# Optimization experiments

Measured on AMD Instinct MI355X. Metric: run time of the kernel, lower is better.

The kernel has to match this reference:

```python
import jax, jax.numpy as jnp
import numpy as np

N_HEADS = 16
ROPE_BASE = 10000.0


def _rope_tables(T, head_dim, dtype):
    inv_freq = 1.0 / (ROPE_BASE ** (jnp.arange(0, head_dim, 2, dtype=jnp.float32) / head_dim))
    t = jnp.arange(T, dtype=jnp.float32)
    freqs = jnp.outer(t, inv_freq)              # (T, head_dim/2)
    emb = jnp.concatenate([freqs, freqs], -1)   # (T, head_dim)
    return jnp.cos(emb).astype(dtype), jnp.sin(emb).astype(dtype)


def _rotate_half(x):
    x1, x2 = jnp.split(x, 2, axis=-1)
    return jnp.concatenate([-x2, x1], axis=-1)


def setup_inputs() -> dict:
    key = jax.random.key(0)
    k1, k2, k3 = jax.random.split(key, 3)
    B, T, C = 2, 2048, 2048
    x = jax.random.normal(k1, (B, T, C), dtype=jnp.float32)
    Wqkv = jax.random.normal(k2, (C, 3 * C), dtype=jnp.float32) * (1.0 / np.sqrt(C))
    Wproj = jax.random.normal(k3, (C, C), dtype=jnp.float32) * (1.0 / np.sqrt(C))
    return {"x": x, "Wqkv": Wqkv, "Wproj": Wproj}


def reference(x, Wqkv, Wproj):
    B, T, C = x.shape
    H = N_HEADS
    D = C // H
    qkv = jnp.einsum('btc,cd->btd', x, Wqkv)            # (B,T,3C)
    q, k, v = jnp.split(qkv, 3, axis=-1)
    # (B,T,C) -> (B,H,T,D)
    q = q.reshape(B, T, H, D).transpose(0, 2, 1, 3)
    k = k.reshape(B, T, H, D).transpose(0, 2, 1, 3)
    v = v.reshape(B, T, H, D).transpose(0, 2, 1, 3)
    cos, sin = _rope_tables(T, D, x.dtype)              # (T,D) each
    q = q * cos + _rotate_half(q) * sin
    k = k * cos + _rotate_half(k) * sin
    scale = 1.0 / jnp.sqrt(jnp.asarray(D, x.dtype))
    att = jnp.einsum('bhqd,bhkd->bhqk', q, k) * scale   # (B,H,T,T)
    causal = jnp.tril(jnp.ones((T, T), dtype=bool))
    att = jnp.where(causal, att, jnp.asarray(-jnp.inf, att.dtype))
    att = jax.nn.softmax(att, axis=-1)
    y = jnp.einsum('bhqk,bhkd->bhqd', att, v)           # (B,H,T,D)
    y = y.transpose(0, 2, 1, 3).reshape(B, T, C)
    return jnp.einsum('btc,cd->btd', y, Wproj)
```

## Files before the change

### kernel.cpp

```cpp
#include <hip/hip_runtime.h>
#include <stdint.h>

#define T_SEQ 2048
#define NH 16
#define HD 128
#define CC 2048
#define N3 6144
#define MM 4096

typedef short bf16x8 __attribute__((ext_vector_type(8)));
typedef float f32x4 __attribute__((ext_vector_type(4)));
typedef float f32x16 __attribute__((ext_vector_type(16)));
typedef unsigned int u32x4 __attribute__((ext_vector_type(4)));

__device__ __forceinline__ unsigned short f2bf(float f) {
  unsigned int u = __float_as_uint(f);
  u += 0x7FFF + ((u >> 16) & 1);
  return (unsigned short)(u >> 16);
}
__device__ __forceinline__ float bf2f(unsigned short h) {
  return __uint_as_float(((unsigned int)h) << 16);
}
__device__ __forceinline__ unsigned int cvt_pk_bf16(float lo, float hi) {
  unsigned int r;
  asm("v_cvt_pk_bf16_f32 %0, %1, %2" : "=v"(r) : "v"(lo), "v"(hi));
  return r;
}

__global__ __launch_bounds__(256) void k_transpose_cvt(const float* __restrict__ in,
                                                       unsigned short* __restrict__ out,
                                                       int K, int N) {
  __shared__ float tile[32][33];
  int k0 = blockIdx.x * 32;
  int n0 = blockIdx.y * 32;
  int tx = threadIdx.x & 31, ty = threadIdx.x >> 5;
  #pragma unroll
  for (int r = ty; r < 32; r += 8)
    tile[r][tx] = in[(size_t)(k0 + r) * N + n0 + tx];
  __syncthreads();
  #pragma unroll
  for (int r = ty; r < 32; r += 8)
    out[(size_t)(n0 + r) * K + k0 + tx] = f2bf(tile[tx][r]);
}

__global__ __launch_bounds__(256) void k_cvt(const float* __restrict__ in,
                                             unsigned short* __restrict__ out, int n4) {
  int i = blockIdx.x * 256 + threadIdx.x;
  if (i >= n4) return;
  float4 v = ((const float4*)in)[i];
  ushort4 o;
  o.x = f2bf(v.x); o.y = f2bf(v.y); o.z = f2bf(v.z); o.w = f2bf(v.w);
  ((ushort4*)out)[i] = o;
}

template<int NJ, int EPI, int MMAJ>
__global__ __launch_bounds__(512, 1) void k_gemm8(const unsigned short* __restrict__ A,
                                                  const unsigned short* __restrict__ Bt,
                                                  float* __restrict__ C,
                                                  unsigned short* __restrict__ qo,
                                                  unsigned short* __restrict__ ko,
                                                  unsigned short* __restrict__ vo,
                                                  int M, int N, int K) {
  constexpr int BU = NJ / 2;
  constexpr int DSTRIDE = (1 + BU) * 16384;
  extern __shared__ __align__(16) char lds[];
  const int tid = threadIdx.x;
  const int lane = tid & 63;
  const int lr = lane & 15, lg = lane >> 4;
  const int wave = tid >> 6;
  const int wm = wave >> 2, wn = wave & 3;
  const int nwg = gridDim.x;
  const int bid = blockIdx.x;
  const int wg = (bid & 7) * (nwg >> 3) + (bid >> 3);
  const int GX = M >> 7;
  const int GN = N / (NJ * 64);
  const int mt = MMAJ ? (wg % GX) : (wg / GN);
  const int nt = MMAJ ? (wg / GX) : (wg % GN);
  const int m0 = mt * 128, n0 = nt * NJ * 64;
  const int NT = K >> 6;

  auto STAGE = [&](int d, int op, int h, int t) {
    const unsigned short* src = op ? Bt : A;
    const int r0 = (op ? n0 + h * 128 : m0);
    const int kc = t * 64;
    char* base = lds + d * DSTRIDE + op * 16384 + h * 16384;
    #pragma unroll
    for (int l = 0; l < 2; ++l) {
      int p = (l * 512 + tid) * 16;
      int qq = p ^ (((p >> 7) & 7) << 4);
      const unsigned short* g = src + (size_t)(r0 + (qq >> 7)) * K + kc + ((qq & 127) >> 1);
      __builtin_amdgcn_global_load_lds(
          (const __attribute__((address_space(1))) void*)g,
          (__attribute__((address_space(3))) void*)(base + (l * 512 + (tid & 448)) * 16),
          16, 0, 0);
    }
  };
  auto RD = [&](int d, int op, int row, int kb) -> bf16x8 {
    const char* base = lds + d * DSTRIDE + op * 16384;
    int p = row * 128 + kb;
    p ^= ((p >> 7) & 7) << 4;
    return *(const bf16x8*)(base + p);
  };

  f32x4 acc[4][NJ];
  #pragma unroll
  for (int i = 0; i < 4; ++i)
    #pragma unroll
    for (int j = 0; j < NJ; ++j) acc[i][j] = (f32x4){0.f, 0.f, 0.f, 0.f};

  bf16x8 bfrg[NJ][2];

#define GPH(D, MI, READB, DOST, SD, SO, SH, ST, VM)                                      \
  {                                                                                      \
    if (READB) {                                                                         \
      _Pragma("unroll")                                                                  \
      for (int nj = 0; nj < NJ; ++nj)                                                    \
        _Pragma("unroll")                                                                \
        for (int ks = 0; ks < 2; ++ks)                                                   \
          bfrg[nj][ks] = RD(D, 1, wn * NJ * 16 + nj * 16 + lr, ks * 64 + lg * 16);       \
    }                                                                                    \
    bf16x8 af[2];                                                                        \
    _Pragma("unroll")                                                                    \
    for (int ks = 0; ks < 2; ++ks)                                                       \
      af[ks] = RD(D, 0, wm * 64 + (MI) * 16 + lr, ks * 64 + lg * 16);                    \
    if (DOST) STAGE(SD, SO, SH, ST);                                                     \
    __builtin_amdgcn_s_barrier();                                                        \
    asm volatile("s_waitcnt lgkmcnt(0)" ::: "memory");                                   \
    __builtin_amdgcn_s_setprio(1);                                                       \
    _Pragma("unroll")                                                                    \
    for (int nj = 0; nj < NJ; ++nj)                                                      \
      _Pragma("unroll")                                                                  \
      for (int ks = 0; ks < 2; ++ks)                                                     \
        acc[MI][nj] = __builtin_amdgcn_mfma_f32_16x16x32_bf16(af[ks], bfrg[nj][ks], acc[MI][nj], 0, 0, 0); \
    __builtin_amdgcn_s_setprio(0);                                                       \
    if ((VM) == 6) asm volatile("s_waitcnt vmcnt(6)" ::: "memory");                      \
    if ((VM) == 4) asm volatile("s_waitcnt vmcnt(4)" ::: "memory");                      \
    __builtin_amdgcn_s_barrier();                                                        \
  }

#define GPM(D, MIB, READB, VM, ...)                                                      \
  {                                                                                      \
    if (READB) {                                                                         \
      _Pragma("unroll")                                                                  \
      for (int nj = 0; nj < NJ; ++nj)                                                    \
        _Pragma("unroll")                                                                \
        for (int ks = 0; ks < 2; ++ks)                                                   \
          bfrg[nj][ks] = RD(D, 1, wn * NJ * 16 + nj * 16 + lr, ks * 64 + lg * 16);       \
    }                                                                                    \
    bf16x8 af2[2][2];                                                                    \
    _Pragma("unroll")                                                                    \
    for (int mm = 0; mm < 2; ++mm)                                                       \
      _Pragma("unroll")                                                                  \
      for (int ks = 0; ks < 2; ++ks)                                                     \
        af2[mm][ks] = RD(D, 0, wm * 64 + (MIB + mm) * 16 + lr, ks * 64 + lg * 16);       \
    __VA_ARGS__                                                                          \
    __builtin_amdgcn_s_barrier();                                                        \
    asm volatile("s_waitcnt lgkmcnt(0)" ::: "memory");                                   \
    __builtin_amdgcn_s_setprio(1);                                                       \
    _Pragma("unroll")                                                                    \
    for (int mm = 0; mm < 2; ++mm)                                                       \
      _Pragma("unroll")                                                                  \
      for (int nj = 0; nj < NJ; ++nj)                                                    \
        _Pragma("unroll")                                                                \
        for (int ks = 0; ks < 2; ++ks)                                                   \
          acc[MIB + mm][nj] = __builtin_amdgcn_mfma_f32_16x16x32_bf16(af2[mm][ks], bfrg[nj][ks], acc[MIB + mm][nj], 0, 0, 0); \
    __builtin_amdgcn_s_setprio(0);                                                       \
    if ((VM) == 4) asm volatile("s_waitcnt vmcnt(4)" ::: "memory");                      \
    if ((VM) == 2) asm volatile("s_waitcnt vmcnt(2)" ::: "memory");                      \
    __builtin_amdgcn_s_barrier();                                                        \
  }

  const int t1 = NT > 1 ? 1 : 0;
  #pragma unroll
  for (int h = 0; h < BU; ++h) STAGE(0, 1, h, 0);
  STAGE(0, 0, 0, 0);
  #pragma unroll
  for (int h = 0; h < BU; ++h) STAGE(1, 1, h, t1);
  if (NJ == 6) asm volatile("s_waitcnt vmcnt(6)" ::: "memory");
  else         asm volatile("s_waitcnt vmcnt(4)" ::: "memory");
  __builtin_amdgcn_s_barrier();

  for (int it = 0; it < (NT >> 1); ++it) {
    const int tb  = 2 * it + 1;
    const int ta1 = min(2 * it + 2, NT - 1);
    const int tb1 = min(2 * it + 3, NT - 1);
    if constexpr (NJ == 6) {
      GPH(0, 0, true,  true, 1, 0, 0, tb,  -1)
      GPH(0, 1, false, true, 0, 1, 0, ta1, -1)
      GPH(0, 2, false, true, 0, 1, 1, ta1, -1)
      GPH(0, 3, false, true, 0, 1, 2, ta1,  6)
      GPH(1, 0, true,  true, 0, 0, 0, ta1, -1)
      GPH(1, 1, false, true, 1, 1, 0, tb1, -1)
      GPH(1, 2, false, true, 1, 1, 1, tb1, -1)
      GPH(1, 3, false, true, 1, 1, 2, tb1,  6)
    } else {
      GPM(0, 0, true,  -1, STAGE(1, 0, 0, tb);)
      GPM(0, 2, false,  2, STAGE(0, 1, 0, ta1);)
      GPM(1, 0, true,  -1, STAGE(0, 1, 1, ta1); STAGE(0, 0, 0, ta1);)
      GPM(1, 2, false,  4, STAGE(1, 1, 0, tb1); STAGE(1, 1, 1, tb1);)
    }
  }
#undef GPH
#undef GPM

  #pragma unroll
  for (int mi = 0; mi < 4; ++mi) {
    #pragma unroll
    for (int nj = 0; nj < NJ; ++nj) {
      #pragma unroll
      for (int j = 0; j < 4; ++j) {
        int m = m0 + wm * 64 + mi * 16 + lg * 4 + j;
        int n = n0 + wn * NJ * 16 + nj * 16 + lr;
        float val = acc[mi][nj][j];
        if (EPI == 0) {
          C[(size_t)m * N + n] = val;
        } else {
          int which = n >> 11, cc = n & 2047;
          int h = cc >> 7, d = cc & 127;
          int b = m >> 11, t = m & 2047;
          unsigned short* dst = which == 0 ? qo : (which == 1 ? ko : vo);
          dst[(((size_t)(b * NH + h)) * T_SEQ + t) * HD + d] = f2bf(val);
        }
      }
    }
  }
}

__global__ __launch_bounds__(256) void k_rope(unsigned short* __restrict__ q,
                                              unsigned short* __restrict__ k) {
  int i = blockIdx.x * 256 + threadIdx.x;
  int d = i & 63;
  int t = (i >> 6) & (T_SEQ - 1);
  int bh = i >> 17;
  float invf = exp2f((float)(-2 * d) * (13.287712379549449f / 128.f));
  float ang = (float)t * invf;
  float c = cosf(ang), s = sinf(ang);
  size_t base = ((size_t)bh * T_SEQ + t) * HD + d;
  const float scale = 0.12751741562076117f;
  float q1 = bf2f(q[base]), q2 = bf2f(q[base + 64]);
  q[base]      = f2bf((q1 * c - q2 * s) * scale);
  q[base + 64] = f2bf((q2 * c + q1 * s) * scale);
  float k1 = bf2f(k[base]), k2 = bf2f(k[base + 64]);
  k[base]      = f2bf(k1 * c - k2 * s);
  k[base + 64] = f2bf(k2 * c + k1 * s);
}

__global__ __launch_bounds__(256) void k_transpose_v(const unsigned short* __restrict__ in,
                                                     unsigned short* __restrict__ out) {
  __shared__ unsigned short tile[32][33];
  int bh = blockIdx.z;
  int t0 = blockIdx.x * 32, d0 = blockIdx.y * 32;
  int tx = threadIdx.x & 31, ty = threadIdx.x >> 5;
  const unsigned short* src = in + (size_t)bh * T_SEQ * HD;
  unsigned short* dst = out + (size_t)bh * HD * T_SEQ;
  #pragma unroll
  for (int r = ty; r < 32; r += 8)
    tile[r][tx] = src[(size_t)(t0 + r) * HD + d0 + tx];
  __syncthreads();
  #pragma unroll
  for (int r = ty; r < 32; r += 8)
    dst[(size_t)(d0 + r) * T_SEQ + t0 + tx] = tile[tx][r];
}

__global__ __launch_bounds__(256, 2) void k_attn(const unsigned short* __restrict__ Q,
                                                 const unsigned short* __restrict__ K,
                                                 const unsigned short* __restrict__ Vt,
                                                 unsigned short* __restrict__ Y) {
  extern __shared__ __align__(16) char alds[];
  char* Kls = alds;
  char* Vls = alds + 32768;
  const int id = blockIdx.x;
  const int sub = id & 255;
  const int bh = sub & 31;
  const int qtl = (id < 256) ? (15 - (sub >> 5)) : (sub >> 5);
  const int b = bh >> 4, h = bh & 15;
  const int tid = threadIdx.x, wv = tid >> 6, lane = tid & 63;
  const int l31 = lane & 31, hh = lane >> 5;
  const int q0 = qtl * 128;
  const int jtmax = 2 * qtl + 1;
  const int qglob = q0 + wv * 32 + l31;
  const unsigned short* Qb = Q + (size_t)bh * T_SEQ * HD;
  const unsigned short* Kb = K + (size_t)bh * T_SEQ * HD;
  const unsigned short* Vb = Vt + (size_t)bh * HD * T_SEQ;

  auto STAGEK = [&](int tk, int s) {
    char* base = Kls + s * 16384;
    #pragma unroll
    for (int ch = 0; ch < 4; ++ch) {
      int p = (ch * 256 + tid) * 16;
      int q = p ^ (((p >> 8) & 7) << 4);
      const unsigned short* g = Kb + (size_t)(tk + (q >> 8)) * HD + ((q & 255) >> 1);
      __builtin_amdgcn_global_load_lds(
          (const __attribute__((address_space(1))) void*)g,
          (__attribute__((address_space(3))) void*)(base + (ch * 256 + (tid & 192)) * 16),
          16, 0, 0);
    }
  };
  auto STAGEV = [&](int tk, int s) {
    char* base = Vls + s * 16384;
    #pragma unroll
    for (int ch = 0; ch < 4; ++ch) {
      int p = (ch * 256 + tid) * 16;
      int q = p ^ (((p >> 7) & 7) << 4);
      const unsigned short* g = Vb + (size_t)(q >> 7) * T_SEQ + tk + ((q & 127) >> 1);
      __builtin_amdgcn_global_load_lds(
          (const __attribute__((address_space(1))) void*)g,
          (__attribute__((address_space(3))) void*)(base + (ch * 256 + (tid & 192)) * 16),
          16, 0, 0);
    }
  };

  bf16x8 qfr[8];
  #pragma unroll
  for (int c = 0; c < 8; ++c)
    qfr[c] = *(const bf16x8*)(Qb + (size_t)qglob * HD + c * 16 + hh * 8);

  f32x16 oacc[4];
  #pragma unroll
  for (int dt = 0; dt < 4; ++dt)
    #pragma unroll
    for (int r = 0; r < 16; ++r) oacc[dt][r] = 0.f;
  float mrun = -1e30f, lrun = 0.f;
  bf16x8 paP0, paP1, paP2, paP3;

#define PV_BLOCK(VBASE_)                                                                 \
  {                                                                                      \
    const char* vb_ = (VBASE_);                                                          \
    __builtin_amdgcn_s_setprio(1);                                                       \
    _Pragma("unroll")                                                                    \
    for (int dt = 0; dt < 4; ++dt) {                                                     \
      _Pragma("unroll")                                                                  \
      for (int c = 0; c < 4; ++c) {                                                      \
        bf16x8 pz = (c == 0) ? paP0 : ((c == 1) ? paP1 : ((c == 2) ? paP2 : paP3));      \
        int row_ = dt * 32 + l31;                                                        \
        int byte_ = (row_ * 128 + c * 32 + hh * 16) ^ ((row_ & 7) << 4);                 \
        bf16x8 vf = *(const bf16x8*)(vb_ + byte_);                                       \
        oacc[dt] = __builtin_amdgcn_mfma_f32_32x32x16_bf16(pz, vf, oacc[dt], 0, 0, 0);   \
      }                                                                                  \
    }                                                                                    \
    __builtin_amdgcn_s_setprio(0);                                                       \
  }

#define MAKE_PA(c, dst)                                                                  \
  {                                                                                      \
    int base_ = ((c) >> 1) * 8 + ((c) & 1) * 4;                                          \
    unsigned int s0 = hh == 0 ? pk[base_ + 2] : pk[base_ + 0];                           \
    unsigned int s1 = hh == 0 ? pk[base_ + 3] : pk[base_ + 1];                           \
    unsigned int r0 = __shfl_xor((int)s0, 32);                                           \
    unsigned int r1 = __shfl_xor((int)s1, 32);                                           \
    u32x4 f;                                                                             \
    f[0] = hh == 0 ? pk[base_ + 0] : r0;                                                 \
    f[1] = hh == 0 ? pk[base_ + 1] : r1;                                                 \
    f[2] = hh == 0 ? r0 : pk[base_ + 2];                                                 \
    f[3] = hh == 0 ? r1 : pk[base_ + 3];                                                 \
    dst = *(bf16x8*)&f;                                                                  \
  }

  STAGEK(0, 0); STAGEV(0, 0);
  asm volatile("s_waitcnt vmcnt(0)" ::: "memory");
  __syncthreads();

  for (int jt = 0; jt <= jtmax; ++jt) {
    const int kcur = jt & 1;
    const int vnext = (jt + 1) % 3;
    const int vprev = (jt + 2) % 3;
    if (jt < jtmax) { STAGEK((jt + 1) * 64, kcur ^ 1); STAGEV((jt + 1) * 64, vnext); }

    f32x16 sacc[2];
    #pragma unroll
    for (int t = 0; t < 2; ++t)
      #pragma unroll
      for (int r = 0; r < 16; ++r) sacc[t][r] = 0.f;
    {
      const char* kbase = Kls + kcur * 16384;
      __builtin_amdgcn_s_setprio(1);
      #pragma unroll
      for (int s = 0; s < 8; ++s) {
        #pragma unroll
        for (int t = 0; t < 2; ++t) {
          int row = t * 32 + l31;
          int byte = (row * 256 + s * 32 + hh * 16) ^ ((row & 7) << 4);
          bf16x8 kf = *(const bf16x8*)(kbase + byte);
          sacc[t] = __builtin_amdgcn_mfma_f32_32x32x16_bf16(kf, qfr[s], sacc[t], 0, 0, 0);
        }
      }
      __builtin_amdgcn_s_setprio(0);
    }

    if (jt >= 2 * qtl) {
      #pragma unroll
      for (int t = 0; t < 2; ++t)
        #pragma unroll
        for (int r = 0; r < 16; ++r) {
          int kg = jt * 64 + t * 32 + (r & 3) + 8 * (r >> 2) + 4 * hh;
          if (kg > qglob) sacc[t][r] = -1e30f;
        }
    }

    if (jt > 0) PV_BLOCK(Vls + vprev * 16384)

    float pmax = sacc[0][0];
    #pragma unroll
    for (int r = 1; r < 16; ++r) pmax = fmaxf(pmax, sacc[0][r]);
    #pragma unroll
    for (int r = 0; r < 16; ++r) pmax = fmaxf(pmax, sacc[1][r]);
    pmax = fmaxf(pmax, __shfl_xor(pmax, 32));

    if (__any(pmax > mrun + 8.0f)) {
      float mnew = fmaxf(mrun, pmax);
      float osc = exp2f(mrun - mnew);
      lrun *= osc;
      mrun = mnew;
      #pragma unroll
      for (int r = 0; r < 16; ++r) {
        int qr = (r & 3) + 8 * (r >> 2) + 4 * hh;
        float sr = __shfl(osc, qr);
        #pragma unroll
        for (int dt = 0; dt < 4; ++dt) oacc[dt][r] *= sr;
      }
    }

    unsigned int pk[16];
    float rsum = 0.f;
    #pragma unroll
    for (int t = 0; t < 2; ++t)
      #pragma unroll
      for (int i = 0; i < 8; ++i) {
        float p0 = exp2f(sacc[t][2 * i] - mrun);
        float p1 = exp2f(sacc[t][2 * i + 1] - mrun);
        rsum += p0 + p1;
        pk[t * 8 + i] = cvt_pk_bf16(p0, p1);
      }
    rsum += __shfl_xor(rsum, 32);
    lrun += rsum;

    MAKE_PA(0, paP0)
    MAKE_PA(1, paP1)
    MAKE_PA(2, paP2)
    MAKE_PA(3, paP3)

    asm volatile("s_waitcnt vmcnt(0)" ::: "memory");
    __syncthreads();
  }

  PV_BLOCK(Vls + (jtmax % 3) * 16384)

  float linv = 1.0f / lrun;
  #pragma unroll
  for (int r = 0; r < 16; ++r) {
    int qr = (r & 3) + 8 * (r >> 2) + 4 * hh;
    float li = __shfl(linv, qr);
    int qg = q0 + wv * 32 + qr;
    size_t base = ((size_t)b * T_SEQ + qg) * CC + h * HD;
    #pragma unroll
    for (int dt = 0; dt < 4; ++dt)
      Y[base + dt * 32 + l31] = f2bf(oacc[dt][r] * li);
  }
#undef PV_BLOCK
#undef MAKE_PA
}

extern "C" void kernel_launch(void* const* d_in, const int* in_sizes, int n_in,
                              void* d_out, int out_size, void* d_ws, size_t ws_size,
                              hipStream_t stream) {
  const float* x     = (const float*)d_in[0];
  const float* Wqkv  = (const float*)d_in[1];
  const float* Wproj = (const float*)d_in[2];
  float* out = (float*)d_out;
  char* ws = (char*)d_ws;
  const size_t MB = 1024 * 1024;
  unsigned short* WqkvT  = (unsigned short*)(ws + 0);
  unsigned short* vt     = (unsigned short*)(ws + 0);
  unsigned short* WprojT = (unsigned short*)(ws + 24 * MB);
  unsigned short* xb     = (unsigned short*)(ws + 32 * MB);
  unsigned short* y      = xb;
  unsigned short* q      = (unsigned short*)(ws + 48 * MB);
  unsigned short* k      = (unsigned short*)(ws + 64 * MB);
  unsigned short* v      = (unsigned short*)(ws + 80 * MB);

  k_transpose_cvt<<<dim3(CC / 32, N3 / 32), 256, 0, stream>>>(Wqkv, WqkvT, CC, N3);
  k_transpose_cvt<<<dim3(CC / 32, CC / 32), 256, 0, stream>>>(Wproj, WprojT, CC, CC);
  k_cvt<<<(MM * CC / 4) / 256, 256, 0, stream>>>(x, xb, MM * CC / 4);
  k_gemm8<6, 1, 1><<<dim3((MM / 128) * (N3 / 384)), 512, 131072, stream>>>(
      xb, WqkvT, nullptr, q, k, v, MM, N3, CC);
  k_rope<<<(32 * T_SEQ * 64) / 256, 256, 0, stream>>>(q, k);
  k_transpose_v<<<dim3(T_SEQ / 32, HD / 32, 32), 256, 0, stream>>>(v, vt);
  k_attn<<<dim3(512), 256, 81920, stream>>>(q, k, vt, y);
  k_gemm8<4, 0, 0><<<dim3((MM / 128) * (CC / 256)), 512, 98304, stream>>>(
      y, WprojT, out, nullptr, nullptr, nullptr, MM, CC, CC);
}
```

Baseline: 267.0 us.

## Split KV tiles across two wave groups per attention block and merge

The attention kernel grows to 512 threads per block. Two groups of four waves each take alternating 64-key tiles (even and odd) for the same 128 queries, so each block's serial KV loop is half as long. Each group keeps its own online-softmax state, and the two partial results are merged through LDS at the end. To support this, K/V staging moves to a 4-slot ring with 128KB of LDS, and the previous software pipelining that overlapped PV with the next QK tile is dropped in favour of a straight QK, softmax, PV sequence. The risks are lower overlap inside a wave, a block-wide barrier every iteration across 8 waves, and extra LDS traffic for the final merge.

```diff
diff --git a/kernel.cpp b/kernel.cpp
--- a/kernel.cpp
+++ b/kernel.cpp
@@ -262,23 +262,23 @@
     dst[(size_t)(d0 + r) * T_SEQ + t0 + tx] = tile[tx][r];
 }
 
-__global__ __launch_bounds__(256, 2) void k_attn(const unsigned short* __restrict__ Q,
+__global__ __launch_bounds__(512, 1) void k_attn(const unsigned short* __restrict__ Q,
                                                  const unsigned short* __restrict__ K,
                                                  const unsigned short* __restrict__ Vt,
                                                  unsigned short* __restrict__ Y) {
   extern __shared__ __align__(16) char alds[];
   char* Kls = alds;
-  char* Vls = alds + 32768;
+  char* Vls = alds + 65536;
   const int id = blockIdx.x;
-  const int sub = id & 255;
-  const int bh = sub & 31;
-  const int qtl = (id < 256) ? (15 - (sub >> 5)) : (sub >> 5);
+  const int bh = id & 31;
+  const int qtl = 15 - (id >> 5);
   const int b = bh >> 4, h = bh & 15;
   const int tid = threadIdx.x, wv = tid >> 6, lane = tid & 63;
   const int l31 = lane & 31, hh = lane >> 5;
+  const int par = wv >> 2;
+  const int wq = wv & 3;
   const int q0 = qtl * 128;
-  const int jtmax = 2 * qtl + 1;
-  const int qglob = q0 + wv * 32 + l31;
+  const int qglob = q0 + wq * 32 + l31;
   const unsigned short* Qb = Q + (size_t)bh * T_SEQ * HD;
   const unsigned short* Kb = K + (size_t)bh * T_SEQ * HD;
   const unsigned short* Vb = Vt + (size_t)bh * HD * T_SEQ;
@@ -286,26 +286,26 @@
   auto STAGEK = [&](int tk, int s) {
     char* base = Kls + s * 16384;
     #pragma unroll
-    for (int ch = 0; ch < 4; ++ch) {
-      int p = (ch * 256 + tid) * 16;
+    for (int ch = 0; ch < 2; ++ch) {
+      int p = (ch * 512 + tid) * 16;
       int q = p ^ (((p >> 8) & 7) << 4);
       const unsigned short* g = Kb + (size_t)(tk + (q >> 8)) * HD + ((q & 255) >> 1);
       __builtin_amdgcn_global_load_lds(
           (const __attribute__((address_space(1))) void*)g,
-          (__attribute__((address_space(3))) void*)(base + (ch * 256 + (tid & 192)) * 16),
+          (__attribute__((address_space(3))) void*)(base + (ch * 512 + (tid & 448)) * 16),
           16, 0, 0);
     }
   };
   auto STAGEV = [&](int tk, int s) {
     char* base = Vls + s * 16384;
     #pragma unroll
-    for (int ch = 0; ch < 4; ++ch) {
-      int p = (ch * 256 + tid) * 16;
+    for (int ch = 0; ch < 2; ++ch) {
+      int p = (ch * 512 + tid) * 16;
       int q = p ^ (((p >> 7) & 7) << 4);
       const unsigned short* g = Vb + (size_t)(q >> 7) * T_SEQ + tk + ((q & 127) >> 1);
       __builtin_amdgcn_global_load_lds(
           (const __attribute__((address_space(1))) void*)g,
-          (__attribute__((address_space(3))) void*)(base + (ch * 256 + (tid & 192)) * 16),
+          (__attribute__((address_space(3))) void*)(base + (ch * 512 + (tid & 448)) * 16),
           16, 0, 0);
     }
   };
@@ -321,50 +321,19 @@
     #pragma unroll
     for (int r = 0; r < 16; ++r) oacc[dt][r] = 0.f;
   float mrun = -1e30f, lrun = 0.f;
-  bf16x8 paP0, paP1, paP2, paP3;
-
-#define PV_BLOCK(VBASE_)                                                                 \
-  {                                                                                      \
-    const char* vb_ = (VBASE_);                                                          \
-    __builtin_amdgcn_s_setprio(1);                                                       \
-    _Pragma("unroll")                                                                    \
-    for (int dt = 0; dt < 4; ++dt) {                                                     \
-      _Pragma("unroll")                                                                  \
-      for (int c = 0; c < 4; ++c) {                                                      \
-        bf16x8 pz = (c == 0) ? paP0 : ((c == 1) ? paP1 : ((c == 2) ? paP2 : paP3));      \
-        int row_ = dt * 32 + l31;                                                        \
-        int byte_ = (row_ * 128 + c * 32 + hh * 16) ^ ((row_ & 7) << 4);                 \
-        bf16x8 vf = *(const bf16x8*)(vb_ + byte_);                                       \
-        oacc[dt] = __builtin_amdgcn_mfma_f32_32x32x16_bf16(pz, vf, oacc[dt], 0, 0, 0);   \
-      }                                                                                  \
-    }                                                                                    \
-    __builtin_amdgcn_s_setprio(0);                                                       \
-  }
-
-#define MAKE_PA(c, dst)                                                                  \
-  {                                                                                      \
-    int base_ = ((c) >> 1) * 8 + ((c) & 1) * 4;                                          \
-    unsigned int s0 = hh == 0 ? pk[base_ + 2] : pk[base_ + 0];                           \
-    unsigned int s1 = hh == 0 ? pk[base_ + 3] : pk[base_ + 1];                           \
-    unsigned int r0 = __shfl_xor((int)s0, 32);                                           \
-    unsigned int r1 = __shfl_xor((int)s1, 32);                                           \
-    u32x4 f;                                                                             \
-    f[0] = hh == 0 ? pk[base_ + 0] : r0;                                                 \
-    f[1] = hh == 0 ? pk[base_ + 1] : r1;                                                 \
-    f[2] = hh == 0 ? r0 : pk[base_ + 2];                                                 \
-    f[3] = hh == 0 ? r1 : pk[base_ + 3];                                                 \
-    dst = *(bf16x8*)&f;                                                                  \
-  }
 
   STAGEK(0, 0); STAGEV(0, 0);
+  STAGEK(64, 1); STAGEV(64, 1);
   asm volatile("s_waitcnt vmcnt(0)" ::: "memory");
   __syncthreads();
 
-  for (int jt = 0; jt <= jtmax; ++jt) {
-    const int kcur = jt & 1;
-    const int vnext = (jt + 1) % 3;
-    const int vprev = (jt + 2) % 3;
-    if (jt < jtmax) { STAGEK((jt + 1) * 64, kcur ^ 1); STAGEV((jt + 1) * 64, vnext); }
+  for (int u = 0; u <= qtl; ++u) {
+    if (u < qtl) {
+      STAGEK((2 * u + 2) * 64, (2 * u + 2) & 3); STAGEV((2 * u + 2) * 64, (2 * u + 2) & 3);
+      STAGEK((2 * u + 3) * 64, (2 * u + 3) & 3); STAGEV((2 * u + 3) * 64, (2 * u + 3) & 3);
+    }
+    const int jt = 2 * u + par;
+    const int slot = jt & 3;
 
     f32x16 sacc[2];
     #pragma unroll
@@ -372,19 +341,22 @@
       #pragma unroll
       for (int r = 0; r < 16; ++r) sacc[t][r] = 0.f;
     {
-      const char* kbase = Kls + kcur * 16384;
-      __builtin_amdgcn_s_setprio(1);
-      #pragma unroll
-      for (int s = 0; s < 8; ++s) {
+      const char* kbase = Kls + slot * 16384;
+      #pragma unroll
+      for (int t = 0; t < 2; ++t) {
+        bf16x8 kf8[8];
         #pragma unroll
-        for (int t = 0; t < 2; ++t) {
+        for (int s = 0; s < 8; ++s) {
           int row = t * 32 + l31;
           int byte = (row * 256 + s * 32 + hh * 16) ^ ((row & 7) << 4);
-          bf16x8 kf = *(const bf16x8*)(kbase + byte);
-          sacc[t] = __builtin_amdgcn_mfma_f32_32x32x16_bf16(kf, qfr[s], sacc[t], 0, 0, 0);
+          kf8[s] = *(const bf16x8*)(kbase + byte);
         }
+        __builtin_amdgcn_s_setprio(1);
+        #pragma unroll
+        for (int s = 0; s < 8; ++s)
+          sacc[t] = __builtin_amdgcn_mfma_f32_32x32x16_bf16(kf8[s], qfr[s], sacc[t], 0, 0, 0);
+        __builtin_amdgcn_s_setprio(0);
       }
-      __builtin_amdgcn_s_setprio(0);
     }
 
     if (jt >= 2 * qtl) {
@@ -396,8 +368,6 @@
           if (kg > qglob) sacc[t][r] = -1e30f;
         }
     }
-
-    if (jt > 0) PV_BLOCK(Vls + vprev * 16384)
 
     float pmax = sacc[0][0];
     #pragma unroll
@@ -434,30 +404,78 @@
     rsum += __shfl_xor(rsum, 32);
     lrun += rsum;
 
-    MAKE_PA(0, paP0)
-    MAKE_PA(1, paP1)
-    MAKE_PA(2, paP2)
-    MAKE_PA(3, paP3)
+    bf16x8 pa[4];
+    #pragma unroll
+    for (int c = 0; c < 4; ++c) {
+      int base = (c >> 1) * 8 + (c & 1) * 4;
+      unsigned int s0 = hh == 0 ? pk[base + 2] : pk[base + 0];
+      unsigned int s1 = hh == 0 ? pk[base + 3] : pk[base + 1];
+      unsigned int r0 = __shfl_xor((int)s0, 32);
+      unsigned int r1 = __shfl_xor((int)s1, 32);
+      u32x4 f;
+      f[0] = hh == 0 ? pk[base + 0] : r0;
+      f[1] = hh == 0 ? pk[base + 1] : r1;
+      f[2] = hh == 0 ? r0 : pk[base + 2];
+      f[3] = hh == 0 ? r1 : pk[base + 3];
+      pa[c] = *(bf16x8*)&f;
+    }
+
+    {
+      const char* vbase = Vls + slot * 16384;
+      __builtin_amdgcn_s_setprio(1);
+      #pragma unroll
+      for (int dt = 0; dt < 4; ++dt) {
+        #pragma unroll
+        for (int c = 0; c < 4; ++c) {
+          int row = dt * 32 + l31;
+          int byte = (row * 128 + c * 32 + hh * 16) ^ ((row & 7) << 4);
+          bf16x8 vf = *(const bf16x8*)(vbase + byte);
+          oacc[dt] = __builtin_amdgcn_mfma_f32_32x32x16_bf16(pa[c], vf, oacc[dt], 0, 0, 0);
+        }
+      }
+      __builtin_amdgcn_s_setprio(0);
+    }
 
     asm volatile("s_waitcnt vmcnt(0)" ::: "memory");
     __syncthreads();
   }
 
-  PV_BLOCK(Vls + (jtmax % 3) * 16384)
-
-  float linv = 1.0f / lrun;
-  #pragma unroll
-  for (int r = 0; r < 16; ++r) {
-    int qr = (r & 3) + 8 * (r >> 2) + 4 * hh;
-    float li = __shfl(linv, qr);
-    int qg = q0 + wv * 32 + qr;
-    size_t base = ((size_t)b * T_SEQ + qg) * CC + h * HD;
+  float* obuf  = (float*)alds;
+  float* mlbuf = (float*)(alds + 65536);
+  if (par == 1) {
+    mlbuf[(wq * 64 + lane) * 2 + 0] = mrun;
+    mlbuf[(wq * 64 + lane) * 2 + 1] = lrun;
+    float* ob = obuf + wq * 4096;
     #pragma unroll
     for (int dt = 0; dt < 4; ++dt)
-      Y[base + dt * 32 + l31] = f2bf(oacc[dt][r] * li);
-  }
-#undef PV_BLOCK
-#undef MAKE_PA
+      #pragma unroll
+      for (int r = 0; r < 16; ++r)
+        ob[(dt * 16 + r) * 64 + lane] = oacc[dt][r];
+  }
+  __syncthreads();
+  if (par == 0) {
+    float mo = mlbuf[(wq * 64 + lane) * 2 + 0];
+    float lo = mlbuf[(wq * 64 + lane) * 2 + 1];
+    float mm = fmaxf(mrun, mo);
+    float se = exp2f(mrun - mm), so = exp2f(mo - mm);
+    float lt = lrun * se + lo * so;
+    float linv = 1.0f / lt;
+    const float* ob = obuf + wq * 4096;
+    #pragma unroll
+    for (int r = 0; r < 16; ++r) {
+      int qr = (r & 3) + 8 * (r >> 2) + 4 * hh;
+      float se_r = __shfl(se, qr);
+      float so_r = __shfl(so, qr);
+      float li_r = __shfl(linv, qr);
+      int qg = q0 + wq * 32 + qr;
+      size_t base = ((size_t)b * T_SEQ + qg) * CC + h * HD;
+      #pragma unroll
+      for (int dt = 0; dt < 4; ++dt) {
+        float oo = ob[(dt * 16 + r) * 64 + lane];
+        Y[base + dt * 32 + l31] = f2bf((oacc[dt][r] * se_r + oo * so_r) * li_r);
+      }
+    }
+  }
 }
 
 extern "C" void kernel_launch(void* const* d_in, const int* in_sizes, int n_in,
@@ -485,7 +503,7 @@
       xb, WqkvT, nullptr, q, k, v, MM, N3, CC);
   k_rope<<<(32 * T_SEQ * 64) / 256, 256, 0, stream>>>(q, k);
   k_transpose_v<<<dim3(T_SEQ / 32, HD / 32, 32), 256, 0, stream>>>(v, vt);
-  k_attn<<<dim3(512), 256, 81920, stream>>>(q, k, vt, y);
+  k_attn<<<dim3(512), 512, 131072, stream>>>(q, k, vt, y);
   k_gemm8<4, 0, 0><<<dim3((MM / 128) * (CC / 256)), 512, 98304, stream>>>(
       y, WprojT, out, nullptr, nullptr, nullptr, MM, CC, CC);
 }
```

Result: faster. 261.1 us (-2.2%).
